# Kernel tuning notes

Hardware: AMD Instinct MI355X
Metric: run time of the kernel (lower is better)

## Reference

```python
import jax, jax.numpy as jnp
import numpy as np

DIM = 384
HEADS = 6
HEAD_DIM = DIM // HEADS
HIDDEN = 4 * DIM
EPS = 1e-5


def layer_norm(x, w, b):
    m = jnp.mean(x, axis=-1, keepdims=True)
    v = jnp.mean((x - m) ** 2, axis=-1, keepdims=True)
    return (x - m) * jax.lax.rsqrt(v + EPS) * w + b


def setup_inputs() -> dict:
    key = jax.random.key(0)
    ks = jax.random.split(key, 8)
    B, N = 2, 4096
    s_in = 1.0 / np.sqrt(DIM)
    s_h = 1.0 / np.sqrt(HIDDEN)
    return {
        "x": jax.random.normal(ks[0], (B, N, DIM), dtype=jnp.float32),
        "qkv_w": jax.random.normal(ks[1], (3 * DIM, DIM), dtype=jnp.float32) * s_in,
        "proj_w": jax.random.normal(ks[2], (DIM, DIM), dtype=jnp.float32) * s_in,
        "proj_b": jnp.zeros((DIM,), dtype=jnp.float32),
        "ln1_w": jnp.ones((DIM,), dtype=jnp.float32),
        "ln1_b": jnp.zeros((DIM,), dtype=jnp.float32),
        "ln2_w": jnp.ones((DIM,), dtype=jnp.float32),
        "ln2_b": jnp.zeros((DIM,), dtype=jnp.float32),
        "fc1_w": jax.random.normal(ks[3], (HIDDEN, DIM), dtype=jnp.float32) * s_in,
        "fc1_b": jnp.zeros((HIDDEN,), dtype=jnp.float32),
        "fc2_w": jax.random.normal(ks[4], (DIM, HIDDEN), dtype=jnp.float32) * s_h,
        "fc2_b": jnp.zeros((DIM,), dtype=jnp.float32),
    }


def reference(x, qkv_w, proj_w, proj_b, ln1_w, ln1_b, ln2_w, ln2_b,
              fc1_w, fc1_b, fc2_w, fc2_b):
    B, N, C = x.shape
    scale = HEAD_DIM ** (-0.5)

    # pre-norm attention
    y = layer_norm(x, ln1_w, ln1_b)
    qkv = (y @ qkv_w.T).reshape(B, N, 3, HEADS, HEAD_DIM)
    qkv = jnp.transpose(qkv, (2, 0, 3, 1, 4))  # [3, B, H, N, D]
    q, k, v = qkv[0], qkv[1], qkv[2]
    attn = jnp.einsum("bhnd,bhmd->bhnm", q, k) * scale  # [B,H,N,N]
    attn = jax.nn.softmax(attn, axis=-1)
    y = jnp.einsum("bhnm,bhmd->bhnd", attn, v)
    y = jnp.transpose(y, (0, 2, 1, 3)).reshape(B, N, C)
    y = y @ proj_w.T + proj_b

    # residual + LN2 + MLP (faithful to source: output = 2 * mlp(ln2(x + y)))
    x = x + y
    x = layer_norm(x, ln2_w, ln2_b)
    h = jax.nn.gelu(x @ fc1_w.T + fc1_b, approximate=False)
    x = h @ fc2_w.T + fc2_b
    x = x + x
    return x
```

## Files before the change

kernel.cpp:

```cpp
#include <hip/hip_runtime.h>
#include <hip/hip_bf16.h>

#define DIM 384
#define HEADS 6
#define HD 64
#define HIDDEN 1536
#define SEQ 4096
#define BATCH 2
#define NTOK (BATCH*SEQ)
#define QKVN (3*DIM)

typedef __attribute__((ext_vector_type(4))) float f32x4;
typedef __attribute__((ext_vector_type(16))) float f32x16;
typedef __attribute__((ext_vector_type(8))) short s16x8;
typedef __attribute__((ext_vector_type(4))) unsigned int u32x4;

__device__ __forceinline__ ushort f2bf(float f) {
    union { float f; unsigned u; } v; v.f = f;
    unsigned r = v.u + 0x7FFF + ((v.u >> 16) & 1);
    return (ushort)(r >> 16);
}
__device__ __forceinline__ float bf2f(ushort b) {
    union { unsigned u; float f; } v; v.u = ((unsigned)b) << 16;
    return v.f;
}
__device__ __forceinline__ unsigned cvtpk(float lo, float hi) {
    unsigned r;
    asm("v_cvt_pk_bf16_f32 %0, %1, %2" : "=v"(r) : "v"(lo), "v"(hi));
    return r;
}
__device__ __forceinline__ void pl32swap(unsigned& a, unsigned& b) {
    asm volatile("v_permlane32_swap_b32 %0, %1" : "+v"(a), "+v"(b));
}
__device__ __forceinline__ void g2l(const ushort* g, ushort* s) {
    __builtin_amdgcn_global_load_lds((const __attribute__((address_space(1))) void*)g,
                                     (__attribute__((address_space(3))) void*)s, 16, 0, 0);
}

__global__ void cvt4_kernel(const float4* __restrict__ s0, ushort* __restrict__ d0, int n0,
                            const float4* __restrict__ s1, ushort* __restrict__ d1, int n1,
                            const float4* __restrict__ s2, ushort* __restrict__ d2, int n2,
                            const float4* __restrict__ s3, ushort* __restrict__ d3, int n3) {
    int i = blockIdx.x * 256 + threadIdx.x;
    const float4* s; ushort* d; int k = i;
    if (i < n0) { s = s0; d = d0; }
    else { k -= n0; if (k < n1) { s = s1; d = d1; }
        else { k -= n1; if (k < n2) { s = s2; d = d2; }
            else { k -= n2; if (k >= n3) return; s = s3; d = d3; } } }
    float4 v = s[k];
    ushort4 o; o.x = f2bf(v.x); o.y = f2bf(v.y); o.z = f2bf(v.z); o.w = f2bf(v.w);
    *(ushort4*)(d + (size_t)k * 4) = o;
}

__global__ __launch_bounds__(256) void ln_kernel(const float* __restrict__ x,
        const float* __restrict__ w, const float* __restrict__ b,
        ushort* __restrict__ y) {
    int l = threadIdx.x & 63;
    int row = blockIdx.x * 4 + (threadIdx.x >> 6);
    const float* xr = x + (size_t)row * DIM;
    float v[6], s = 0.f, s2 = 0.f;
#pragma unroll
    for (int i = 0; i < 6; ++i) { v[i] = xr[l + 64*i]; s += v[i]; s2 += v[i]*v[i]; }
#pragma unroll
    for (int d = 1; d < 64; d <<= 1) { s += __shfl_xor(s, d); s2 += __shfl_xor(s2, d); }
    float mean = s * (1.f/DIM);
    float var  = s2 * (1.f/DIM) - mean*mean;
    float rstd = rsqrtf(var + 1e-5f);
    ushort* yr = y + (size_t)row * DIM;
#pragma unroll
    for (int i = 0; i < 6; ++i) {
        int c = l + 64*i;
        yr[c] = f2bf((v[i]-mean)*rstd*w[c] + b[c]);
    }
}

template<int EPI, int BN>
__global__ __launch_bounds__(256) void gemm_kernel(
        const ushort* __restrict__ A, const ushort* __restrict__ W,
        const float* __restrict__ bias, const float* __restrict__ resid,
        void* __restrict__ Cout, int M, int N, int K) {
    __shared__ __align__(16) ushort lds_a[128*32];
    __shared__ __align__(16) ushort lds_b[BN*32];
    const int t = threadIdx.x, l = t & 63, wid = t >> 6;
    const int lo = l & 15, lg = l >> 4;
    const int m0 = blockIdx.x * 128, n0 = blockIdx.y * BN;
    constexpr int MI = (BN == 128) ? 4 : 2;
    const int wrow = (BN == 128) ? (wid >> 1) * 64 : wid * 32;
    const int wcol = (BN == 128) ? (wid & 1) * 64 : 0;
    f32x4 acc[MI][4] = {};
    const int srow = l >> 2, scol = (l & 3) * 8;
    const ushort* gA0 = A + (size_t)(m0 + wid*16 + srow) * K + scol;
    const ushort* gA1 = A + (size_t)(m0 + (wid+4)*16 + srow) * K + scol;
    const ushort* gB0 = W + (size_t)(n0 + wid*16 + srow) * K + scol;
    const ushort* gB1 = W + (size_t)(n0 + ((wid+4)*16 % BN) + srow) * K + scol;
    ushort* la0 = &lds_a[wid * 512];
    ushort* la1 = &lds_a[(wid + 4) * 512];
    ushort* lb0 = &lds_b[wid * 512];
    ushort* lb1 = (BN == 128) ? &lds_b[(wid + 4) * 512] : nullptr;

    for (int k0 = 0; k0 < K; k0 += 32) {
        g2l(gA0 + k0, la0);
        g2l(gA1 + k0, la1);
        g2l(gB0 + k0, lb0);
        if constexpr (BN == 128) g2l(gB1 + k0, lb1);
        __syncthreads();
        s16x8 af[MI], bf[4];
#pragma unroll
        for (int mi = 0; mi < MI; ++mi)
            af[mi] = *(const s16x8*)&lds_a[(wrow + mi*16 + lo)*32 + lg*8];
#pragma unroll
        for (int ni = 0; ni < 4; ++ni)
            bf[ni] = *(const s16x8*)&lds_b[(wcol + ni*16 + lo)*32 + lg*8];
#pragma unroll
        for (int mi = 0; mi < MI; ++mi)
#pragma unroll
            for (int ni = 0; ni < 4; ++ni)
                acc[mi][ni] = __builtin_amdgcn_mfma_f32_16x16x32_bf16(af[mi], bf[ni], acc[mi][ni], 0,0,0);
        __syncthreads();
    }
#pragma unroll
    for (int mi = 0; mi < MI; ++mi)
#pragma unroll
    for (int ni = 0; ni < 4; ++ni)
#pragma unroll
    for (int r = 0; r < 4; ++r) {
        int row = m0 + wrow + mi*16 + lg*4 + r;
        int col = n0 + wcol + ni*16 + lo;
        float c = acc[mi][ni][r];
        size_t idx = (size_t)row * N + col;
        if (EPI == 0) {
            ((ushort*)Cout)[idx] = f2bf(c);
        } else if (EPI == 1) {
            ((float*)Cout)[idx] = c + bias[col] + resid[idx];
        } else if (EPI == 2) {
            c += bias[col];
            ((ushort*)Cout)[idx] = f2bf(0.5f * c * (1.f + erff(c * 0.70710678118f)));
        } else {
            ((float*)Cout)[idx] = 2.f * (c + bias[col]);
        }
    }
}

#define PV_STEP(S, MM, CB) do {                                                   \
    unsigned w0 = cvtpk(S[8*MM+0], S[8*MM+1]);                                    \
    unsigned w1 = cvtpk(S[8*MM+2], S[8*MM+3]);                                    \
    unsigned w2 = cvtpk(S[8*MM+4], S[8*MM+5]);                                    \
    unsigned w3 = cvtpk(S[8*MM+6], S[8*MM+7]);                                    \
    pl32swap(w0, w2); pl32swap(w1, w3);                                           \
    u32x4 fw = {w0, w1, w2, w3};                                                  \
    s16x8 pa = __builtin_bit_cast(s16x8, fw);                                     \
    int colb = ((CB) + G*8) ^ swz0;                                               \
    s16x8 vb0 = *(const s16x8*)&lds_v[half][q31][colb];                           \
    s16x8 vb1 = *(const s16x8*)&lds_v[half][32 + q31][colb ^ 32];                 \
    o0 = __builtin_amdgcn_mfma_f32_32x32x16_bf16(pa, vb0, o0, 0,0,0);             \
    o1 = __builtin_amdgcn_mfma_f32_32x32x16_bf16(pa, vb1, o1, 0,0,0);             \
} while (0)

__global__ __launch_bounds__(256, 3) void attn_kernel(const ushort* __restrict__ qkv,
                                                      ushort* __restrict__ out) {
    __shared__ __align__(16) ushort lds_k[2][64][72];
    __shared__ __align__(16) ushort lds_v[2][64][72];
    const int t = threadIdx.x, l = t & 63, wid = t >> 6;
    const int G = l >> 5, q31 = l & 31, half = wid >> 1;
    const int b = blockIdx.y / HEADS, h = blockIdx.y % HEADS;
    const ushort* base = qkv + (size_t)b * SEQ * QKVN + h * HD;
    const int q0 = blockIdx.x * 64 + (wid & 1) * 32;

    const float QSC = 0.1803368801111137f;
    s16x8 qf[4];
#pragma unroll
    for (int dc = 0; dc < 4; ++dc) {
        s16x8 qv = *(const s16x8*)(base + (size_t)(q0 + q31) * QKVN + dc*16 + G*8);
#pragma unroll
        for (int j = 0; j < 8; ++j)
            qv[j] = (short)f2bf(bf2f((ushort)qv[j]) * QSC);
        qf[dc] = qv;
    }

    f32x16 o0 = {}, o1 = {};
    float l_run = 0.f;

    const int u = t & 127, sa = u >> 3, sc = u & 7;
    const ushort* kbase = base + DIM;
    const ushort* vbase = base + 2*DIM;
    const int key0base = half * (SEQ/2);
    const int swz0 = ((q31 >> 3) & 3) << 3;

    s16x8 kreg[4];
#pragma unroll
    for (int p = 0; p < 4; ++p)
        kreg[p] = *(const s16x8*)(kbase + (size_t)(key0base + p*16 + sa) * QKVN + sc*8);

    for (int it = 0; it < 32; ++it) {
        const int key0 = key0base + it*64;
        s16x8 vreg[4];
#pragma unroll
        for (int p = 0; p < 4; ++p)
            vreg[p] = *(const s16x8*)(vbase + (size_t)(key0 + p*16 + sa) * QKVN + sc*8);
        __syncthreads();
#pragma unroll
        for (int p = 0; p < 4; ++p) {
            *(s16x8*)&lds_k[half][p*16 + sa][sc*8] = kreg[p];
            const int colp = (p*16 + sa) ^ ((sc & 3) << 3) ^ ((sc >> 2) << 5);
#pragma unroll
            for (int j = 0; j < 8; ++j)
                lds_v[half][sc*8 + j][colp] = (ushort)vreg[p][j];
        }
        __syncthreads();
        if (it < 31) {
#pragma unroll
            for (int p = 0; p < 4; ++p)
                kreg[p] = *(const s16x8*)(kbase + (size_t)(key0 + 64 + p*16 + sa) * QKVN + sc*8);
        }

        f32x16 st0 = {}, st1 = {};
        __builtin_amdgcn_s_setprio(1);
#pragma unroll
        for (int dc = 0; dc < 4; ++dc) {
            s16x8 kf0 = *(const s16x8*)&lds_k[half][q31][dc*16 + G*8];
            s16x8 kf1 = *(const s16x8*)&lds_k[half][32 + q31][dc*16 + G*8];
            st0 = __builtin_amdgcn_mfma_f32_32x32x16_bf16(kf0, qf[dc], st0, 0,0,0);
            st1 = __builtin_amdgcn_mfma_f32_32x32x16_bf16(kf1, qf[dc], st1, 0,0,0);
        }
        __builtin_amdgcn_s_setprio(0);

        float c0 = 0.f, c1 = 0.f, c2 = 0.f, c3 = 0.f;
#pragma unroll
        for (int r = 0; r < 16; r += 4) {
            st0[r]   = exp2f(st0[r]);   c0 += st0[r];
            st0[r+1] = exp2f(st0[r+1]); c1 += st0[r+1];
            st0[r+2] = exp2f(st0[r+2]); c2 += st0[r+2];
            st0[r+3] = exp2f(st0[r+3]); c3 += st0[r+3];
            st1[r]   = exp2f(st1[r]);   c0 += st1[r];
            st1[r+1] = exp2f(st1[r+1]); c1 += st1[r+1];
            st1[r+2] = exp2f(st1[r+2]); c2 += st1[r+2];
            st1[r+3] = exp2f(st1[r+3]); c3 += st1[r+3];
        }
        l_run += (c0 + c1) + (c2 + c3);

        __builtin_amdgcn_s_setprio(1);
        PV_STEP(st0, 0, 0);
        PV_STEP(st0, 1, 16);
        PV_STEP(st1, 0, 32);
        PV_STEP(st1, 1, 48);
        __builtin_amdgcn_s_setprio(0);
    }

    l_run += __shfl_xor(l_run, 32);

    __syncthreads();
    float* mb = (float*)&lds_k[0][0][0];
    float* ml = (float*)&lds_v[0][0][0];
    if (half == 1) {
#pragma unroll
        for (int r = 0; r < 16; ++r) {
            mb[((wid&1)*2 + 0)*1024 + r*64 + l] = o0[r];
            mb[((wid&1)*2 + 1)*1024 + r*64 + l] = o1[r];
        }
        ml[(wid&1)*64 + l] = l_run;
    }
    __syncthreads();
    if (half == 0) {
        float lt = l_run + ml[(wid&1)*64 + l];
        float inv = 1.0f / lt;
        ushort* ob = out + (size_t)b * SEQ * DIM + h * HD;
#pragma unroll
        for (int r = 0; r < 16; ++r) {
            int qr = (r & 3) + 8*(r >> 2) + 4*G;
            float invr = __shfl(inv, qr);
            float v0 = (o0[r] + mb[((wid&1)*2 + 0)*1024 + r*64 + l]) * invr;
            float v1 = (o1[r] + mb[((wid&1)*2 + 1)*1024 + r*64 + l]) * invr;
            int row = q0 + qr;
            ob[(size_t)row * DIM + q31]      = f2bf(v0);
            ob[(size_t)row * DIM + 32 + q31] = f2bf(v1);
        }
    }
}

extern "C" void kernel_launch(void* const* d_in, const int* in_sizes, int n_in,
                              void* d_out, int out_size, void* d_ws, size_t ws_size,
                              hipStream_t stream) {
    const float* x      = (const float*)d_in[0];
    const float* qkv_w  = (const float*)d_in[1];
    const float* proj_w = (const float*)d_in[2];
    const float* proj_b = (const float*)d_in[3];
    const float* ln1_w  = (const float*)d_in[4];
    const float* ln1_b  = (const float*)d_in[5];
    const float* ln2_w  = (const float*)d_in[6];
    const float* ln2_b  = (const float*)d_in[7];
    const float* fc1_w  = (const float*)d_in[8];
    const float* fc1_b  = (const float*)d_in[9];
    const float* fc2_w  = (const float*)d_in[10];
    const float* fc2_b  = (const float*)d_in[11];
    float* outp = (float*)d_out;

    char* ws = (char*)d_ws;
    size_t off = 0;
    auto alloc = [&](size_t bytes) {
        off = (off + 255) & ~(size_t)255;
        void* p = ws + off;
        off += bytes;
        return p;
    };
    ushort* wq   = (ushort*)alloc((size_t)QKVN * DIM * 2);
    ushort* wp   = (ushort*)alloc((size_t)DIM * DIM * 2);
    ushort* w1   = (ushort*)alloc((size_t)HIDDEN * DIM * 2);
    ushort* w2   = (ushort*)alloc((size_t)DIM * HIDDEN * 2);
    ushort* y1   = (ushort*)alloc((size_t)NTOK * DIM * 2);
    ushort* qkvb = (ushort*)alloc((size_t)NTOK * QKVN * 2);
    ushort* ao   = (ushort*)alloc((size_t)NTOK * DIM * 2);
    float*  res  = (float*) alloc((size_t)NTOK * DIM * 4);
    ushort* y2   = (ushort*)alloc((size_t)NTOK * DIM * 2);
    ushort* hb   = (ushort*)alloc((size_t)NTOK * HIDDEN * 2);

    const int n0 = QKVN*DIM/4, n1 = DIM*DIM/4, n2 = HIDDEN*DIM/4, n3 = DIM*HIDDEN/4;
    cvt4_kernel<<<(n0+n1+n2+n3 + 255)/256, 256, 0, stream>>>(
        (const float4*)qkv_w, wq, n0, (const float4*)proj_w, wp, n1,
        (const float4*)fc1_w, w1, n2, (const float4*)fc2_w, w2, n3);

    ln_kernel<<<NTOK/4, 256, 0, stream>>>(x, ln1_w, ln1_b, y1);
    gemm_kernel<0,128><<<dim3(NTOK/128, QKVN/128), 256, 0, stream>>>(y1, wq, nullptr, nullptr, qkvb, NTOK, QKVN, DIM);
    attn_kernel<<<dim3(SEQ/64, BATCH*HEADS), 256, 0, stream>>>(qkvb, ao);
    gemm_kernel<1,64><<<dim3(NTOK/128, DIM/64), 256, 0, stream>>>(ao, wp, proj_b, x, res, NTOK, DIM, DIM);
    ln_kernel<<<NTOK/4, 256, 0, stream>>>(res, ln2_w, ln2_b, y2);
    gemm_kernel<2,128><<<dim3(NTOK/128, HIDDEN/128), 256, 0, stream>>>(y2, w1, fc1_b, nullptr, hb, NTOK, HIDDEN, DIM);
    gemm_kernel<3,64><<<dim3(NTOK/128, DIM/64), 256, 0, stream>>>(hb, w2, fc2_b, nullptr, outp, NTOK, DIM, HIDDEN);
}
```

Baseline: 270.3 us.

## Double-buffer GEMM LDS tiles and prefetch V alongside K in attention

The GEMM kernel now keeps two LDS buffers and issues the global-to-LDS loads for the next K-tile before computing on the current one, removing one barrier per k-step and overlapping memory latency with MFMA work. The attention kernel now prefetches V register tiles one iteration ahead together with K, so V loads no longer stall at the top of each iteration. This doubles GEMM LDS usage, which may lower occupancy, and adds register pressure in the attention loop. The gB1 pointer no longer wraps with a modulo for BN=64, but it is only used when BN is 128.

```diff
diff --git a/kernel.cpp b/kernel.cpp
--- a/kernel.cpp
+++ b/kernel.cpp
@@ -79,8 +79,8 @@
         const ushort* __restrict__ A, const ushort* __restrict__ W,
         const float* __restrict__ bias, const float* __restrict__ resid,
         void* __restrict__ Cout, int M, int N, int K) {
-    __shared__ __align__(16) ushort lds_a[128*32];
-    __shared__ __align__(16) ushort lds_b[BN*32];
+    __shared__ __align__(16) ushort lds_a[2][128*32];
+    __shared__ __align__(16) ushort lds_b[2][BN*32];
     const int t = threadIdx.x, l = t & 63, wid = t >> 6;
     const int lo = l & 15, lg = l >> 4;
     const int m0 = blockIdx.x * 128, n0 = blockIdx.y * BN;
@@ -92,32 +92,49 @@
     const ushort* gA0 = A + (size_t)(m0 + wid*16 + srow) * K + scol;
     const ushort* gA1 = A + (size_t)(m0 + (wid+4)*16 + srow) * K + scol;
     const ushort* gB0 = W + (size_t)(n0 + wid*16 + srow) * K + scol;
-    const ushort* gB1 = W + (size_t)(n0 + ((wid+4)*16 % BN) + srow) * K + scol;
-    ushort* la0 = &lds_a[wid * 512];
-    ushort* la1 = &lds_a[(wid + 4) * 512];
-    ushort* lb0 = &lds_b[wid * 512];
-    ushort* lb1 = (BN == 128) ? &lds_b[(wid + 4) * 512] : nullptr;
-
-    for (int k0 = 0; k0 < K; k0 += 32) {
-        g2l(gA0 + k0, la0);
-        g2l(gA1 + k0, la1);
-        g2l(gB0 + k0, lb0);
-        if constexpr (BN == 128) g2l(gB1 + k0, lb1);
+    const ushort* gB1 = W + (size_t)(n0 + (wid+4)*16 + srow) * K + scol;
+
+#define STAGE(BUF, K0) do {                                               \
+    g2l(gA0 + (K0), &lds_a[BUF][wid * 512]);                              \
+    g2l(gA1 + (K0), &lds_a[BUF][(wid + 4) * 512]);                        \
+    g2l(gB0 + (K0), &lds_b[BUF][wid * 512]);                              \
+    if constexpr (BN == 128) g2l(gB1 + (K0), &lds_b[BUF][(wid + 4) * 512]);\
+} while (0)
+
+#define COMPUTE(BUF) do {                                                 \
+    s16x8 af[MI], bfr[4];                                                 \
+    _Pragma("unroll")                                                     \
+    for (int mi = 0; mi < MI; ++mi)                                       \
+        af[mi] = *(const s16x8*)&lds_a[BUF][(wrow + mi*16 + lo)*32 + lg*8];\
+    _Pragma("unroll")                                                     \
+    for (int ni = 0; ni < 4; ++ni)                                        \
+        bfr[ni] = *(const s16x8*)&lds_b[BUF][(wcol + ni*16 + lo)*32 + lg*8];\
+    _Pragma("unroll")                                                     \
+    for (int mi = 0; mi < MI; ++mi)                                       \
+        _Pragma("unroll")                                                 \
+        for (int ni = 0; ni < 4; ++ni)                                    \
+            acc[mi][ni] = __builtin_amdgcn_mfma_f32_16x16x32_bf16(af[mi], bfr[ni], acc[mi][ni], 0,0,0);\
+} while (0)
+
+    const int NT = K / 32;
+    STAGE(0, 0);
+    asm volatile("s_waitcnt vmcnt(0)");
+    __syncthreads();
+    for (int tt = 0; tt < NT; tt += 2) {
+        if (tt + 1 < NT) STAGE(1, (tt + 1) * 32);
+        COMPUTE(0);
+        asm volatile("s_waitcnt vmcnt(0)");
         __syncthreads();
-        s16x8 af[MI], bf[4];
-#pragma unroll
-        for (int mi = 0; mi < MI; ++mi)
-            af[mi] = *(const s16x8*)&lds_a[(wrow + mi*16 + lo)*32 + lg*8];
-#pragma unroll
-        for (int ni = 0; ni < 4; ++ni)
-            bf[ni] = *(const s16x8*)&lds_b[(wcol + ni*16 + lo)*32 + lg*8];
-#pragma unroll
-        for (int mi = 0; mi < MI; ++mi)
-#pragma unroll
-            for (int ni = 0; ni < 4; ++ni)
-                acc[mi][ni] = __builtin_amdgcn_mfma_f32_16x16x32_bf16(af[mi], bf[ni], acc[mi][ni], 0,0,0);
-        __syncthreads();
-    }
+        if (tt + 2 < NT) STAGE(0, (tt + 2) * 32);
+        COMPUTE(1);
+        if (tt + 2 < NT) {
+            asm volatile("s_waitcnt vmcnt(0)");
+            __syncthreads();
+        }
+    }
+#undef STAGE
+#undef COMPUTE
+
 #pragma unroll
     for (int mi = 0; mi < MI; ++mi)
 #pragma unroll
@@ -186,17 +203,15 @@
     const int key0base = half * (SEQ/2);
     const int swz0 = ((q31 >> 3) & 3) << 3;
 
-    s16x8 kreg[4];
-#pragma unroll
-    for (int p = 0; p < 4; ++p)
+    s16x8 kreg[4], vreg[4];
+#pragma unroll
+    for (int p = 0; p < 4; ++p) {
         kreg[p] = *(const s16x8*)(kbase + (size_t)(key0base + p*16 + sa) * QKVN + sc*8);
+        vreg[p] = *(const s16x8*)(vbase + (size_t)(key0base + p*16 + sa) * QKVN + sc*8);
+    }
 
     for (int it = 0; it < 32; ++it) {
         const int key0 = key0base + it*64;
-        s16x8 vreg[4];
-#pragma unroll
-        for (int p = 0; p < 4; ++p)
-            vreg[p] = *(const s16x8*)(vbase + (size_t)(key0 + p*16 + sa) * QKVN + sc*8);
         __syncthreads();
 #pragma unroll
         for (int p = 0; p < 4; ++p) {
@@ -209,8 +224,10 @@
         __syncthreads();
         if (it < 31) {
 #pragma unroll
-            for (int p = 0; p < 4; ++p)
+            for (int p = 0; p < 4; ++p) {
                 kreg[p] = *(const s16x8*)(kbase + (size_t)(key0 + 64 + p*16 + sa) * QKVN + sc*8);
+                vreg[p] = *(const s16x8*)(vbase + (size_t)(key0 + 64 + p*16 + sa) * QKVN + sc*8);
+            }
         }
 
         f32x16 st0 = {}, st1 = {};
```

After: 290.8 us. +7.6%, slower.
